# Performance work log

Hardware: AMD Instinct MI355X
Metric: run time of the kernel (lower is better)

## Reference

```python
import jax, jax.numpy as jnp
import numpy as np

NB_CODE = 1024
CODE_DIM = 64
N, T = 32, 8192


def setup_inputs() -> dict:
    key = jax.random.key(0)
    k1, k2 = jax.random.split(key)
    x = jax.random.normal(k1, (N, T, CODE_DIM), dtype=jnp.float32)
    codebook = jax.random.normal(k2, (NB_CODE, CODE_DIM), dtype=jnp.float32)
    return {"x": x, "codebook": codebook}


def reference(x, codebook):
    # x: [N, T, C] with C == code_dim == encdec_dim -> no projection, no transpose
    n, t, c = x.shape
    nb_code = codebook.shape[0]
    xf = x.reshape(-1, c)  # [NT, C]

    dist = (
        jnp.sum(xf * xf, axis=-1, keepdims=True)
        - 2.0 * (xf @ codebook.T)
        + jnp.sum(codebook * codebook, axis=-1)[None, :]
    )
    # eval-mode gumbel_sample(-dist) == argmax(-dist) == argmin(dist)
    code_idx = jnp.argmin(dist, axis=-1)  # [NT] int32

    # dequantize: embedding gather
    x_d = codebook[code_idx]  # [NT, C]

    # compute_perplexity (no-grad in original): one-hot scatter counts
    counts = jnp.zeros((nb_code,), dtype=xf.dtype).at[code_idx].add(1.0)
    prob = counts / jnp.sum(counts)
    perplexity = jnp.exp(-jnp.sum(prob * jnp.log(prob + 1e-7)))

    # commitment loss: mse(x, detach(x_d))
    commit_loss = jnp.mean(jnp.square(xf - jax.lax.stop_gradient(x_d)))

    # straight-through estimator
    x_out = xf + jax.lax.stop_gradient(x_d - xf)
    x_out = x_out.reshape(n, t, c)
    return x_out, commit_loss, perplexity
```

## Files before the change

### kernel.cpp

```cpp
#include <hip/hip_runtime.h>
#include <cfloat>
#include <cmath>

#define NB_CODE 1024
#define CODE_DIM 64
#define NROWS (32 * 8192)
#define NTC ((size_t)NROWS * CODE_DIM)
#define TAU 0.03f

typedef __attribute__((ext_vector_type(8))) short short8;
typedef __attribute__((ext_vector_type(8))) _Float16 half8;
typedef __attribute__((ext_vector_type(4))) float f32x4;

#define W_LOSS 1024
#define W_FLAGCNT 1025
#define W_CNORM 1028
#define W_CBP 2052
#define W_FLAGLIST 67588

__device__ inline float unmask6(float v) {
    return __uint_as_float(__float_as_uint(v) & 0xFFFFFFC0u);
}

__global__ void prep_kernel(const float* __restrict__ cb, float* __restrict__ ws) {
    int j = blockIdx.x * blockDim.x + threadIdx.x;
    if (j >= NB_CODE) return;
    float* cnorm = ws + W_CNORM;
    half8* cbp = (half8*)(ws + W_CBP);
    const int t = j >> 4, li = j & 15;

    float c2v[CODE_DIM];
    const float4* c4 = reinterpret_cast<const float4*>(cb + (size_t)j * CODE_DIM);
    float s = 0.f;
#pragma unroll
    for (int q = 0; q < 16; ++q) {
        float4 v = c4[q];
        float e[4] = {v.x, v.y, v.z, v.w};
#pragma unroll
        for (int u = 0; u < 4; ++u) {
            s = fmaf(e[u], e[u], s);
            c2v[q * 4 + u] = -2.f * e[u];
        }
    }
    cnorm[j] = s;

#pragma unroll
    for (int f = 0; f < 2; ++f) {
#pragma unroll
        for (int lg = 0; lg < 4; ++lg) {
            half8 h8, l8;
#pragma unroll
            for (int i = 0; i < 8; ++i) {
                float c2 = c2v[32 * f + 8 * lg + i];
                _Float16 hb = (_Float16)c2;
                h8[i] = hb;
                l8[i] = (_Float16)(c2 - (float)hb);
            }
            cbp[(size_t)(t * 4 + f) * 64 + lg * 16 + li] = h8;
            cbp[(size_t)(t * 4 + 2 + f) * 64 + lg * 16 + li] = l8;
        }
    }
}

__global__ __launch_bounds__(512, 4) void vq_mfma_kernel(
    const float* __restrict__ x, const float* __restrict__ cb,
    float* __restrict__ ws, float* __restrict__ out, unsigned int flag_cap)
{
    __shared__ half8 sB[2][2048];
    __shared__ float scn[NB_CODE];
    __shared__ int lds_j[512];

    const int tid = threadIdx.x;
    const int w = tid >> 6, lane = tid & 63;
    const int lg = lane >> 4;
    const int li = lane & 15;
    const int wavebase = blockIdx.x * 512 + w * 64;

    const float* cnorm_g = ws + W_CNORM;
    const half8* cbp_v = (const half8*)(ws + W_CBP);
    unsigned int* counts = (unsigned int*)ws;
    float* loss_sum = ws + W_LOSS;
    unsigned int* flagcnt = (unsigned int*)ws + W_FLAGCNT;
    unsigned int* flaglist = (unsigned int*)ws + W_FLAGLIST;

    half8 xh[4][2];
    float x2sum = 0.f;
#pragma unroll
    for (int rt = 0; rt < 4; ++rt) {
        const float* xr = x + (size_t)(wavebase + rt * 16 + li) * CODE_DIM;
#pragma unroll
        for (int f = 0; f < 2; ++f) {
            const float4* p = reinterpret_cast<const float4*>(xr + 32 * f + 8 * lg);
            float4 v0 = p[0], v1 = p[1];
            float e[8] = {v0.x, v0.y, v0.z, v0.w, v1.x, v1.y, v1.z, v1.w};
            half8 h8;
#pragma unroll
            for (int i = 0; i < 8; ++i) {
                float xe = e[i];
                x2sum = fmaf(xe, xe, x2sum);
                h8[i] = (_Float16)xe;
            }
            xh[rt][f] = h8;
        }
    }

    for (int i = tid; i < NB_CODE; i += 512) scn[i] = cnorm_g[i];

    float best[4][4], second[4][4];
#pragma unroll
    for (int rt = 0; rt < 4; ++rt)
#pragma unroll
        for (int r = 0; r < 4; ++r) { best[rt][r] = FLT_MAX; second[rt][r] = FLT_MAX; }

#define STAGE(bb, phx)                                                          \
    {                                                                           \
        const half8* gsrc_ = cbp_v + (size_t)(phx) * 2048;                      \
        _Pragma("unroll")                                                       \
        for (int k_ = 0; k_ < 4; ++k_) {                                        \
            const int bidx_ = k_ * 512 + w * 64;                                \
            __builtin_amdgcn_global_load_lds(                                   \
                (const __attribute__((address_space(1))) unsigned int*)(gsrc_ + bidx_ + lane), \
                (__attribute__((address_space(3))) unsigned int*)&sB[bb][bidx_],\
                16, 0, 0);                                                      \
        }                                                                       \
    }

    asm volatile("s_waitcnt vmcnt(0)" ::: "memory");
    __builtin_amdgcn_sched_barrier(0);
    STAGE(0, 0);
    STAGE(1, 1);
    asm volatile("s_waitcnt vmcnt(4) lgkmcnt(0)" ::: "memory");
    __builtin_amdgcn_sched_barrier(0);
    __builtin_amdgcn_s_barrier();

    for (int ph = 0; ph < 8; ++ph) {
        const int b = ph & 1;
        const half8* bufp = sB[b];
#pragma unroll 2
        for (int tl = 0; tl < 8; ++tl) {
            const int T = ph * 8 + tl;
            const int bo = tl * 256 + lane;
            half8 c0 = bufp[bo];
            half8 c1 = bufp[bo + 64];
            half8 c2 = bufp[bo + 128];
            half8 c3 = bufp[bo + 192];
            float cn = scn[T * 16 + li];
            f32x4 ci = {cn, cn, cn, cn};
#pragma unroll
            for (int rt = 0; rt < 4; ++rt) {
                f32x4 acc = __builtin_amdgcn_mfma_f32_16x16x32_f16(xh[rt][0], c0, ci, 0, 0, 0);
                acc = __builtin_amdgcn_mfma_f32_16x16x32_f16(xh[rt][1], c1, acc, 0, 0, 0);
                acc = __builtin_amdgcn_mfma_f32_16x16x32_f16(xh[rt][0], c2, acc, 0, 0, 0);
                acc = __builtin_amdgcn_mfma_f32_16x16x32_f16(xh[rt][1], c3, acc, 0, 0, 0);
#pragma unroll
                for (int r = 0; r < 4; ++r) {
                    float p = __uint_as_float((__float_as_uint(acc[r]) & 0xFFFFFFC0u) | (unsigned)T);
                    second[rt][r] = fminf(second[rt][r], fmaxf(best[rt][r], p));
                    best[rt][r] = fminf(best[rt][r], p);
                }
            }
        }
        asm volatile("s_waitcnt lgkmcnt(0)" ::: "memory");
        __builtin_amdgcn_sched_barrier(0);
        __builtin_amdgcn_s_barrier();
        if (ph < 6) {
            STAGE(b, ph + 2);
            asm volatile("s_waitcnt vmcnt(4)" ::: "memory");
        } else {
            asm volatile("s_waitcnt vmcnt(0)" ::: "memory");
        }
        __builtin_amdgcn_sched_barrier(0);
        __builtin_amdgcn_s_barrier();
    }
#undef STAGE

    int codef[4][4];
#pragma unroll
    for (int rt = 0; rt < 4; ++rt)
#pragma unroll
        for (int r = 0; r < 4; ++r) {
            float b = best[rt][r], s = second[rt][r];
            int code = ((int)(__float_as_uint(b) & 63u) << 4) | li;
#pragma unroll
            for (int m = 1; m <= 8; m <<= 1) {
                float ob = __shfl_xor(b, m, 64);
                float os = __shfl_xor(s, m, 64);
                int   oc = __shfl_xor(code, m, 64);
                s = fminf(fminf(s, os), fmaxf(b, ob));
                bool take = (ob < b) || (ob == b && oc < code);
                if (take) { b = ob; code = oc; }
            }
            best[rt][r] = b; second[rt][r] = s; codef[rt][r] = code;
        }

    float lsum = x2sum;
    if (li == 0) {
#pragma unroll
        for (int rt = 0; rt < 4; ++rt)
#pragma unroll
            for (int r = 0; r < 4; ++r) {
                int rowin = rt * 16 + lg * 4 + r;
                int j = codef[rt][r];
                lds_j[w * 64 + rowin] = j;
                atomicAdd(&counts[j], 1u);
                float bd = unmask6(best[rt][r]);
                lsum += bd;
                if (unmask6(second[rt][r]) - bd <= TAU) {
                    unsigned pos = atomicAdd(flagcnt, 1u);
                    if (pos < flag_cap)
                        flaglist[pos] = ((unsigned)(wavebase + rowin) << 10) | (unsigned)j;
                }
            }
    }
#pragma unroll
    for (int m = 32; m >= 1; m >>= 1) lsum += __shfl_down(lsum, m, 64);
    if (lane == 0) atomicAdd(loss_sum, lsum);

    __syncthreads();

    for (int it = 0; it < 16; ++it) {
        int rowin = it * 4 + lg;
        int j = lds_j[w * 64 + rowin];
        float4 v = *reinterpret_cast<const float4*>(cb + (size_t)j * CODE_DIM + li * 4);
        *reinterpret_cast<float4*>(out + (size_t)(wavebase + rowin) * CODE_DIM + li * 4) = v;
    }
}

__global__ __launch_bounds__(256) void fixup_kernel(
    const float* __restrict__ x, const float* __restrict__ cb,
    float* __restrict__ ws, float* __restrict__ out, unsigned int flag_cap)
{
    unsigned nf = *((unsigned*)ws + W_FLAGCNT);
    if (nf > flag_cap) nf = flag_cap;
    const float* cnorm = ws + W_CNORM;
    unsigned* flaglist = (unsigned*)ws + W_FLAGLIST;
    unsigned* counts = (unsigned*)ws;

    const int lane = threadIdx.x & 63;
    const unsigned wave_id = (blockIdx.x * blockDim.x + threadIdx.x) >> 6;
    const unsigned nwaves = (gridDim.x * blockDim.x) >> 6;

    for (unsigned idx = wave_id; idx < nf; idx += nwaves) {
        unsigned e = flaglist[idx];
        int row = (int)(e >> 10);
        int oldj = (int)(e & 1023u);

        float xr[CODE_DIM];
        const float4* x4 = reinterpret_cast<const float4*>(x + (size_t)row * CODE_DIM);
#pragma unroll
        for (int q = 0; q < 16; ++q) {
            float4 v = x4[q];
            xr[4 * q + 0] = v.x; xr[4 * q + 1] = v.y;
            xr[4 * q + 2] = v.z; xr[4 * q + 3] = v.w;
        }

        float bestv = FLT_MAX; int bj = 0x7fffffff;
        for (int t = 0; t < 16; ++t) {
            int j = lane * 16 + t;
            const float* c = cb + (size_t)j * CODE_DIM;
            float d0 = 0.f, d1 = 0.f, d2 = 0.f, d3 = 0.f;
#pragma unroll
            for (int k = 0; k < CODE_DIM; k += 4) {
                d0 = fmaf(xr[k + 0], c[k + 0], d0);
                d1 = fmaf(xr[k + 1], c[k + 1], d1);
                d2 = fmaf(xr[k + 2], c[k + 2], d2);
                d3 = fmaf(xr[k + 3], c[k + 3], d3);
            }
            float dist = fmaf(-2.f, (d0 + d1) + (d2 + d3), cnorm[j]);
            if (dist < bestv) { bestv = dist; bj = j; }
        }
#pragma unroll
        for (int m = 1; m <= 32; m <<= 1) {
            float ob = __shfl_xor(bestv, m, 64);
            int   oj = __shfl_xor(bj, m, 64);
            bool take = (ob < bestv) || (ob == bestv && oj < bj);
            if (take) { bestv = ob; bj = oj; }
        }

        if (bj != oldj) {
            if (lane < 16) {
                *reinterpret_cast<float4*>(out + (size_t)row * CODE_DIM + lane * 4) =
                    *reinterpret_cast<const float4*>(cb + (size_t)bj * CODE_DIM + lane * 4);
            }
            if (lane == 0) {
                atomicAdd(&counts[bj], 1u);
                atomicAdd(&counts[oldj], (unsigned)-1);
            }
        }
    }
}

__global__ void finalize_kernel(const unsigned int* __restrict__ counts,
                                const float* __restrict__ loss_sum,
                                float* __restrict__ out)
{
    __shared__ float red[NB_CODE];
    int t = threadIdx.x;
    float p = (float)counts[t] / (float)NROWS;
    red[t] = p * logf(p + 1e-7f);
    __syncthreads();
    for (int s = NB_CODE / 2; s > 0; s >>= 1) {
        if (t < s) red[t] += red[t + s];
        __syncthreads();
    }
    if (t == 0) {
        out[NTC + 0] = *loss_sum / (float)NTC;
        out[NTC + 1] = expf(-red[0]);
    }
}

extern "C" void kernel_launch(void* const* d_in, const int* in_sizes, int n_in,
                              void* d_out, int out_size, void* d_ws, size_t ws_size,
                              hipStream_t stream) {
    const float* x  = (const float*)d_in[0];
    const float* cb = (const float*)d_in[1];
    float* out = (float*)d_out;
    float* ws = (float*)d_ws;

    unsigned flag_cap = 0;
    size_t words = ws_size / 4;
    if (words > (size_t)W_FLAGLIST) flag_cap = (unsigned)(words - W_FLAGLIST);
    if (flag_cap > NROWS) flag_cap = NROWS;

    hipMemsetAsync(d_ws, 0, 1028 * sizeof(float), stream);

    prep_kernel<<<NB_CODE / 256, 256, 0, stream>>>(cb, ws);
    vq_mfma_kernel<<<NROWS / 512, 512, 0, stream>>>(x, cb, ws, out, flag_cap);
    fixup_kernel<<<512, 256, 0, stream>>>(x, cb, ws, out, flag_cap);
    finalize_kernel<<<1, NB_CODE, 0, stream>>>((unsigned int*)ws, ws + W_LOSS, out);
}
```

Baseline: 311.7 us.

## Replace LDS-staged codebook pipeline with direct register double-buffered global loads

Drops the shared-memory double buffer fed by global_load_lds, along with its block barriers. Each wave now loads codebook tiles and norms straight from global (L2/L1-cached) into registers, using a two-tile software prefetch. The hi/lo MFMA chain is split into two independent accumulators to shorten the dependency chain. Blocks shrink to 256 threads, and the fixup grid is doubled. The trade is that every wave fetches the whole codebook through the vector cache instead of sharing it via LDS, which raises global/L1 traffic and register use. In exchange it removes the barrier stalls.

```diff
diff --git a/kernel.cpp b/kernel.cpp
--- a/kernel.cpp
+++ b/kernel.cpp
@@ -8,7 +8,6 @@
 #define NTC ((size_t)NROWS * CODE_DIM)
 #define TAU 0.03f
 
-typedef __attribute__((ext_vector_type(8))) short short8;
 typedef __attribute__((ext_vector_type(8))) _Float16 half8;
 typedef __attribute__((ext_vector_type(4))) float f32x4;
 
@@ -62,22 +61,33 @@
     }
 }
 
-__global__ __launch_bounds__(512, 4) void vq_mfma_kernel(
+struct BT { half8 b0, b1, b2, b3; float cn; };
+
+__device__ inline void load_tile(const half8* __restrict__ cbp,
+                                 const float* __restrict__ cnorm,
+                                 int t, int lane, int li, BT& T)
+{
+    const half8* base = cbp + (size_t)t * 4 * 64 + lane;
+    T.b0 = base[0];
+    T.b1 = base[64];
+    T.b2 = base[128];
+    T.b3 = base[192];
+    T.cn = cnorm[t * 16 + li];
+}
+
+__global__ __launch_bounds__(256) void vq_mfma_kernel(
     const float* __restrict__ x, const float* __restrict__ cb,
     float* __restrict__ ws, float* __restrict__ out, unsigned int flag_cap)
 {
-    __shared__ half8 sB[2][2048];
-    __shared__ float scn[NB_CODE];
-    __shared__ int lds_j[512];
-
+    __shared__ int lds_j[4 * 64];
     const int tid = threadIdx.x;
     const int w = tid >> 6, lane = tid & 63;
     const int lg = lane >> 4;
     const int li = lane & 15;
-    const int wavebase = blockIdx.x * 512 + w * 64;
-
-    const float* cnorm_g = ws + W_CNORM;
-    const half8* cbp_v = (const half8*)(ws + W_CBP);
+    const int wavebase = blockIdx.x * 256 + w * 64;
+
+    const float* cnorm = ws + W_CNORM;
+    const half8* cbp = (const half8*)(ws + W_CBP);
     unsigned int* counts = (unsigned int*)ws;
     float* loss_sum = ws + W_LOSS;
     unsigned int* flagcnt = (unsigned int*)ws + W_FLAGCNT;
@@ -104,75 +114,43 @@
         }
     }
 
-    for (int i = tid; i < NB_CODE; i += 512) scn[i] = cnorm_g[i];
-
     float best[4][4], second[4][4];
 #pragma unroll
     for (int rt = 0; rt < 4; ++rt)
 #pragma unroll
         for (int r = 0; r < 4; ++r) { best[rt][r] = FLT_MAX; second[rt][r] = FLT_MAX; }
 
-#define STAGE(bb, phx)                                                          \
-    {                                                                           \
-        const half8* gsrc_ = cbp_v + (size_t)(phx) * 2048;                      \
-        _Pragma("unroll")                                                       \
-        for (int k_ = 0; k_ < 4; ++k_) {                                        \
-            const int bidx_ = k_ * 512 + w * 64;                                \
-            __builtin_amdgcn_global_load_lds(                                   \
-                (const __attribute__((address_space(1))) unsigned int*)(gsrc_ + bidx_ + lane), \
-                (__attribute__((address_space(3))) unsigned int*)&sB[bb][bidx_],\
-                16, 0, 0);                                                      \
-        }                                                                       \
-    }
-
-    asm volatile("s_waitcnt vmcnt(0)" ::: "memory");
-    __builtin_amdgcn_sched_barrier(0);
-    STAGE(0, 0);
-    STAGE(1, 1);
-    asm volatile("s_waitcnt vmcnt(4) lgkmcnt(0)" ::: "memory");
-    __builtin_amdgcn_sched_barrier(0);
-    __builtin_amdgcn_s_barrier();
-
-    for (int ph = 0; ph < 8; ++ph) {
-        const int b = ph & 1;
-        const half8* bufp = sB[b];
-#pragma unroll 2
-        for (int tl = 0; tl < 8; ++tl) {
-            const int T = ph * 8 + tl;
-            const int bo = tl * 256 + lane;
-            half8 c0 = bufp[bo];
-            half8 c1 = bufp[bo + 64];
-            half8 c2 = bufp[bo + 128];
-            half8 c3 = bufp[bo + 192];
-            float cn = scn[T * 16 + li];
-            f32x4 ci = {cn, cn, cn, cn};
-#pragma unroll
-            for (int rt = 0; rt < 4; ++rt) {
-                f32x4 acc = __builtin_amdgcn_mfma_f32_16x16x32_f16(xh[rt][0], c0, ci, 0, 0, 0);
-                acc = __builtin_amdgcn_mfma_f32_16x16x32_f16(xh[rt][1], c1, acc, 0, 0, 0);
-                acc = __builtin_amdgcn_mfma_f32_16x16x32_f16(xh[rt][0], c2, acc, 0, 0, 0);
-                acc = __builtin_amdgcn_mfma_f32_16x16x32_f16(xh[rt][1], c3, acc, 0, 0, 0);
-#pragma unroll
-                for (int r = 0; r < 4; ++r) {
-                    float p = __uint_as_float((__float_as_uint(acc[r]) & 0xFFFFFFC0u) | (unsigned)T);
-                    second[rt][r] = fminf(second[rt][r], fmaxf(best[rt][r], p));
-                    best[rt][r] = fminf(best[rt][r], p);
-                }
-            }
-        }
-        asm volatile("s_waitcnt lgkmcnt(0)" ::: "memory");
-        __builtin_amdgcn_sched_barrier(0);
-        __builtin_amdgcn_s_barrier();
-        if (ph < 6) {
-            STAGE(b, ph + 2);
-            asm volatile("s_waitcnt vmcnt(4)" ::: "memory");
-        } else {
-            asm volatile("s_waitcnt vmcnt(0)" ::: "memory");
-        }
-        __builtin_amdgcn_sched_barrier(0);
-        __builtin_amdgcn_s_barrier();
-    }
-#undef STAGE
+    const f32x4 zero4 = {0.f, 0.f, 0.f, 0.f};
+
+#define CT_TILE(Tt, Tidx)                                                                    \
+    {                                                                                        \
+        f32x4 ci = {Tt.cn, Tt.cn, Tt.cn, Tt.cn};                                             \
+        _Pragma("unroll")                                                                    \
+        for (int rt = 0; rt < 4; ++rt) {                                                     \
+            f32x4 a1 = __builtin_amdgcn_mfma_f32_16x16x32_f16(xh[rt][0], Tt.b0, ci, 0, 0, 0);    \
+            f32x4 a2 = __builtin_amdgcn_mfma_f32_16x16x32_f16(xh[rt][0], Tt.b2, zero4, 0, 0, 0); \
+            a1 = __builtin_amdgcn_mfma_f32_16x16x32_f16(xh[rt][1], Tt.b1, a1, 0, 0, 0);          \
+            a2 = __builtin_amdgcn_mfma_f32_16x16x32_f16(xh[rt][1], Tt.b3, a2, 0, 0, 0);          \
+            _Pragma("unroll")                                                                \
+            for (int r = 0; r < 4; ++r) {                                                    \
+                float d = a1[r] + a2[r];                                                     \
+                float p = __uint_as_float((__float_as_uint(d) & 0xFFFFFFC0u) | (unsigned)(Tidx)); \
+                second[rt][r] = fminf(second[rt][r], fmaxf(best[rt][r], p));                 \
+                best[rt][r] = fminf(best[rt][r], p);                                         \
+            }                                                                                \
+        }                                                                                    \
+    }
+
+    BT A_, B_;
+    load_tile(cbp, cnorm, 0, lane, li, A_);
+    load_tile(cbp, cnorm, 1, lane, li, B_);
+    for (int t = 0; t < 64; t += 2) {
+        CT_TILE(A_, t);
+        load_tile(cbp, cnorm, (t + 2) & 63, lane, li, A_);
+        CT_TILE(B_, t + 1);
+        load_tile(cbp, cnorm, (t + 3) & 63, lane, li, B_);
+    }
+#undef CT_TILE
 
     int codef[4][4];
 #pragma unroll
@@ -325,7 +303,7 @@
     hipMemsetAsync(d_ws, 0, 1028 * sizeof(float), stream);
 
     prep_kernel<<<NB_CODE / 256, 256, 0, stream>>>(cb, ws);
-    vq_mfma_kernel<<<NROWS / 512, 512, 0, stream>>>(x, cb, ws, out, flag_cap);
-    fixup_kernel<<<512, 256, 0, stream>>>(x, cb, ws, out, flag_cap);
+    vq_mfma_kernel<<<NROWS / 256, 256, 0, stream>>>(x, cb, ws, out, flag_cap);
+    fixup_kernel<<<1024, 256, 0, stream>>>(x, cb, ws, out, flag_cap);
     finalize_kernel<<<1, NB_CODE, 0, stream>>>((unsigned int*)ws, ws + W_LOSS, out);
 }
```

New measurement: 280.6 us. -10.0%, faster.
